# Kernel tuning notes

Hardware: AMD Instinct MI355X
Metric: run time of the kernel (lower is better)

Reference implementation:

```python
import jax, jax.numpy as jnp
import numpy as np

B, N, C = 8, 196, 512
NC, H = 10, 8
HD = C // H
SCALE = HD ** -0.5


def setup_inputs() -> dict:
    key = jax.random.key(0)
    ks = jax.random.split(key, 8)
    s = 1.0 / np.sqrt(C)
    return {
        "x": jax.random.normal(ks[0], (B, N, C), jnp.float32),
        "anchors": jax.random.normal(ks[1], (NC, N, C), jnp.float32),
        "weights": jax.random.uniform(ks[2], (B, H, NC), jnp.float32),
        "Wqk": jax.random.normal(ks[3], (C, C), jnp.float32) * s,
        "Wqk2": jax.random.normal(ks[4], (C, C), jnp.float32) * s,
        "Wv": jax.random.normal(ks[5], (C, C), jnp.float32) * s,
        "Wproj": jax.random.normal(ks[6], (C, C), jnp.float32) * s,
        "bproj": jax.random.normal(ks[7], (C,), jnp.float32) * 0.01,
    }


def _heads(t):
    # (..., N, C) -> (..., H, N, HD)
    shp = t.shape[:-2]
    return t.reshape(shp + (t.shape[-2], H, HD)).swapaxes(-3, -2)


def reference(x, anchors, weights, Wqk, Wqk2, Wv, Wproj, bproj):
    v = _heads(x @ Wv)                      # (B, H, N, HD)
    q = _heads(x @ Wqk)[:, None]            # (B, 1, H, N, HD)
    k = _heads(anchors @ Wqk)[None]         # (1, NC, H, N, HD)
    q2 = _heads(x @ Wqk2)[:, None]          # (B, 1, H, N, HD)
    k2 = _heads(anchors @ Wqk2)[None]       # (1, NC, H, N, HD)

    # ReLU-clipped double attention, both (B, NC, H, N, N)
    left_attn = jnp.maximum(-(q @ k.swapaxes(-2, -1)) * SCALE, 0.0)
    right_attn = jnp.maximum((k2 @ q2.swapaxes(-2, -1)) * SCALE, 0.0)

    attn = left_attn @ right_attn           # (B, NC, H, N, N)
    # per-head class-weighted combine: (B,H,NC) x (B,NC,H,N,N) -> (B,H,N,N)
    tmp = jnp.einsum('bhc,bchnm->bhnm', weights, attn)
    out = tmp @ v                           # (B, H, N, HD)
    # NOTE: original torch code reshapes (B,H,N,HD)->(B,N,C) WITHOUT a
    # transpose back; we replicate that exact flatten order.
    out = out.reshape(B, N, C)
    out = out @ Wproj + bproj
    return (out, left_attn)
```

## Files before the change

### kernel.cpp

```cpp
#include <hip/hip_runtime.h>

#define OFF_XB     0u
#define OFF_AB     1605632u
#define OFF_WQKT   3612672u
#define OFF_WQK2T  4136960u
#define OFF_WVT    4661248u
#define OFF_WPROJT 5185536u
#define OFF_XQ     5709824u
#define OFF_XQ2    7315456u
#define OFF_XV     8921088u
#define OFF_AQ     10526720u
#define OFF_AQ2    12533760u
#define OFF_RVT    14540800u
#define OFF_OUT1   35512320u
#define OFF_P      37117952u

typedef __attribute__((ext_vector_type(8))) short bf16x8;
typedef __attribute__((ext_vector_type(4))) float f32x4;
#define MFMA(a, b, c) __builtin_amdgcn_mfma_f32_16x16x32_bf16((a), (b), (c), 0, 0, 0)

__device__ __forceinline__ unsigned short f2bf(float x) {
  unsigned u = __builtin_bit_cast(unsigned, x);
  u += 0x7fffu + ((u >> 16) & 1u);
  return (unsigned short)(u >> 16);
}
__device__ __forceinline__ float bf2f(unsigned short s) {
  return __builtin_bit_cast(float, ((unsigned)s) << 16);
}

__device__ __forceinline__ void barrier_lds() {
  asm volatile("s_waitcnt lgkmcnt(0)" ::: "memory");
  __builtin_amdgcn_s_barrier();
  asm volatile("" ::: "memory");
}

__device__ __forceinline__ void gl_lds16(const void* g, void* l) {
  __builtin_amdgcn_global_load_lds(
      (const __attribute__((address_space(1))) unsigned int*)g,
      (__attribute__((address_space(3))) unsigned int*)l, 16, 0, 0);
}

__device__ __forceinline__ void stage64(const unsigned short* g0, int stride,
                                        unsigned short (*T)[72], int tid, int nrows) {
  int wv = tid >> 6;
  char* base = (char*)&T[0][0];
#pragma unroll
  for (int i = 0; i < 2; i++) {
    int k = i * 256 + tid;
    int r = k / 9, c = k - r * 9;
    if (r < nrows)
      gl_lds16(g0 + (size_t)r * stride + (c << 3), base + (((i << 2) + wv) << 10));
  }
  if (tid < 64) {
    int k = 512 + tid;
    int r = k / 9, c = k - r * 9;
    if (r < nrows)
      gl_lds16(g0 + (size_t)r * stride + (c << 3), base + 8192);
  }
}

__device__ __forceinline__ void stageA_f32(unsigned short (*T)[72], const float* __restrict__ A,
                                           int row0, int M, int k0, int tid) {
  int r = tid >> 2, cs = (tid & 3) << 4;
  float4 f0 = make_float4(0.f, 0.f, 0.f, 0.f), f1 = f0, f2 = f0, f3 = f0;
  if (row0 + r < M) {
    const float* p = A + (size_t)(row0 + r) * 512 + k0 + cs;
    f0 = *(const float4*)p;
    f1 = *(const float4*)(p + 4);
    f2 = *(const float4*)(p + 8);
    f3 = *(const float4*)(p + 12);
  }
  unsigned short s[16] = {f2bf(f0.x), f2bf(f0.y), f2bf(f0.z), f2bf(f0.w),
                          f2bf(f1.x), f2bf(f1.y), f2bf(f1.z), f2bf(f1.w),
                          f2bf(f2.x), f2bf(f2.y), f2bf(f2.z), f2bf(f2.w),
                          f2bf(f3.x), f2bf(f3.y), f2bf(f3.z), f2bf(f3.w)};
  *(uint4*)&T[r][cs] = *(uint4*)s;
  *(uint4*)&T[r][cs + 8] = *(uint4*)(s + 8);
}

__device__ __forceinline__ void vload_T(uint4* va, uint4* vb, const unsigned short* __restrict__ g,
                                        int row0, int nrows, int col0, int tid) {
  int j0 = tid >> 3, d0 = (tid & 7) << 3;
  *va = make_uint4(0, 0, 0, 0);
  *vb = make_uint4(0, 0, 0, 0);
  if (j0 < nrows) *va = *(const uint4*)(g + (size_t)(row0 + j0) * 512 + col0 + d0);
  if (j0 + 32 < nrows) *vb = *(const uint4*)(g + (size_t)(row0 + j0 + 32) * 512 + col0 + d0);
}
__device__ __forceinline__ void vwrite_T(unsigned short T[64][72], uint4 va, uint4 vb, int tid) {
  int j0 = tid >> 3, d0 = (tid & 7) << 3;
  int sw = (tid & 7) << 3;
  unsigned short s[8];
  *(uint4*)s = va;
#pragma unroll
  for (int u = 0; u < 8; u++) T[d0 + u][j0 ^ sw] = s[u];
  *(uint4*)s = vb;
#pragma unroll
  for (int u = 0; u < 8; u++) T[d0 + u][(j0 + 32) ^ sw] = s[u];
}

__global__ __launch_bounds__(256) void pre_kernel(const float* __restrict__ Wqk, const float* __restrict__ Wqk2,
                                                  const float* __restrict__ Wv, const float* __restrict__ Wproj,
                                                  char* __restrict__ ws) {
  __shared__ __align__(16) unsigned short Ls[64][72];
  int tid = threadIdx.x;
  int idx = blockIdx.x;
  int wsel = idx >> 6, t = idx & 63;
  int k0 = (t >> 3) << 6, n0 = (t & 7) << 6;
  const float* W;
  unsigned short* WT;
  switch (wsel) {
    case 0:  W = Wqk;   WT = (unsigned short*)(ws + OFF_WQKT);   break;
    case 1:  W = Wqk2;  WT = (unsigned short*)(ws + OFF_WQK2T);  break;
    case 2:  W = Wv;    WT = (unsigned short*)(ws + OFF_WVT);    break;
    default: W = Wproj; WT = (unsigned short*)(ws + OFF_WPROJT); break;
  }
  {
    int r = tid >> 2, seg = (tid & 3) << 4;
    const float* p = W + (size_t)(k0 + r) * 512 + n0 + seg;
    float4 f0 = *(const float4*)p, f1 = *(const float4*)(p + 4);
    float4 f2 = *(const float4*)(p + 8), f3 = *(const float4*)(p + 12);
    unsigned short s[16] = {f2bf(f0.x), f2bf(f0.y), f2bf(f0.z), f2bf(f0.w),
                            f2bf(f1.x), f2bf(f1.y), f2bf(f1.z), f2bf(f1.w),
                            f2bf(f2.x), f2bf(f2.y), f2bf(f2.z), f2bf(f2.w),
                            f2bf(f3.x), f2bf(f3.y), f2bf(f3.z), f2bf(f3.w)};
    *(uint4*)&Ls[r][seg] = *(uint4*)s;
    *(uint4*)&Ls[r][seg + 8] = *(uint4*)(s + 8);
  }
  __syncthreads();
  {
    int r = tid >> 2, seg = (tid & 3) << 4;
    unsigned short s[16];
#pragma unroll
    for (int u = 0; u < 16; u++) s[u] = Ls[seg + u][r];
    unsigned short* dst = WT + (size_t)(n0 + r) * 512 + k0 + seg;
    *(uint4*)dst = *(uint4*)s;
    *(uint4*)(dst + 8) = *(uint4*)(s + 8);
  }
}

template <int NW>
__device__ __forceinline__ void proj_body(const float* __restrict__ A,
                                          const unsigned short* W0, const unsigned short* W1,
                                          const unsigned short* W2,
                                          unsigned short* O0, unsigned short* O1, unsigned short* O2,
                                          int M, unsigned short (*As)[72], unsigned short (*Wsh)[72]) {
  int row0 = (int)blockIdx.x << 6;
  if (row0 >= M) return;
  int col0 = (int)blockIdx.y << 6;
  int tid = threadIdx.x;
  int w = tid >> 6, lm = tid & 15, lq = (tid >> 4) & 3;
  const unsigned short* WTs[3] = {W0, W1, W2};
  unsigned short* Os[3] = {O0, O1, O2};
  f32x4 acc[NW][4] = {};
  for (int k0 = 0; k0 < 512; k0 += 64) {
    __syncthreads();
    stageA_f32(As, A, row0, M, k0, tid);
#pragma unroll
    for (int ww = 0; ww < NW; ww++)
      stage64(WTs[ww] + (size_t)col0 * 512 + k0, 512,
              (unsigned short(*)[72])&Wsh[ww << 6], tid, 64);
    __syncthreads();
#pragma unroll
    for (int kk = 0; kk < 2; kk++) {
      bf16x8 af[4];
#pragma unroll
      for (int mi = 0; mi < 4; mi++)
        af[mi] = *(const bf16x8*)&As[(mi << 4) + lm][(kk << 5) + (lq << 3)];
#pragma unroll
      for (int ww = 0; ww < NW; ww++) {
        bf16x8 bf = *(const bf16x8*)&Wsh[(ww << 6) + (w << 4) + lm][(kk << 5) + (lq << 3)];
#pragma unroll
        for (int mi = 0; mi < 4; mi++) acc[ww][mi] = MFMA(af[mi], bf, acc[ww][mi]);
      }
    }
  }
  int ncol = col0 + (w << 4) + lm;
#pragma unroll
  for (int ww = 0; ww < NW; ww++)
#pragma unroll
    for (int mi = 0; mi < 4; mi++)
#pragma unroll
      for (int r2 = 0; r2 < 4; r2++) {
        int row = row0 + (mi << 4) + (lq << 2) + r2;
        if (row < M)
          Os[ww][(size_t)row * 512 + ncol] = f2bf(acc[ww][mi][r2]);
      }
}

__global__ __launch_bounds__(256) void proj_combo(const float* __restrict__ x,
                                                  const float* __restrict__ anchors,
                                                  char* __restrict__ ws) {
  __shared__ __align__(16) unsigned short As[64][72];
  __shared__ __align__(16) unsigned short Wsh[192][72];
  const unsigned short* wqkt  = (const unsigned short*)(ws + OFF_WQKT);
  const unsigned short* wqk2t = (const unsigned short*)(ws + OFF_WQK2T);
  const unsigned short* wvt   = (const unsigned short*)(ws + OFF_WVT);
  if (blockIdx.z == 0)
    proj_body<3>(x, wqkt, wqk2t, wvt,
                 (unsigned short*)(ws + OFF_XQ), (unsigned short*)(ws + OFF_XQ2),
                 (unsigned short*)(ws + OFF_XV), 1568, As, Wsh);
  else
    proj_body<2>(anchors, wqkt, wqk2t, nullptr,
                 (unsigned short*)(ws + OFF_AQ), (unsigned short*)(ws + OFF_AQ2),
                 nullptr, 1960, As, Wsh);
}

__global__ __launch_bounds__(256) void final_gemm(const unsigned short* __restrict__ out1,
                                                  const unsigned short* __restrict__ WT,
                                                  const float* __restrict__ bias, float* __restrict__ out) {
  __shared__ __align__(16) unsigned short As[64][72];
  __shared__ __align__(16) unsigned short Ws[64][72];
  int row0 = (int)blockIdx.x << 6;
  int col0 = (int)blockIdx.y << 6;
  int tid = threadIdx.x;
  int w = tid >> 6, lm = tid & 15, lq = (tid >> 4) & 3;
  f32x4 acc[4] = {};
  for (int k0 = 0; k0 < 512; k0 += 64) {
    __syncthreads();
    stage64(out1 + (size_t)row0 * 512 + k0, 512, As, tid, 64);
    stage64(WT + (size_t)col0 * 512 + k0, 512, Ws, tid, 64);
    __syncthreads();
#pragma unroll
    for (int kk = 0; kk < 2; kk++) {
      bf16x8 bf = *(const bf16x8*)&Ws[(w << 4) + lm][(kk << 5) + (lq << 3)];
#pragma unroll
      for (int mi = 0; mi < 4; mi++) {
        bf16x8 af = *(const bf16x8*)&As[(mi << 4) + lm][(kk << 5) + (lq << 3)];
        acc[mi] = MFMA(af, bf, acc[mi]);
      }
    }
  }
  int ncol = col0 + (w << 4) + lm;
  float bv = bias[ncol];
#pragma unroll
  for (int mi = 0; mi < 4; mi++)
#pragma unroll
    for (int r2 = 0; r2 < 4; r2++) {
      int row = row0 + (mi << 4) + (lq << 2) + r2;
      if (row < 1568)
        out[(size_t)row * 512 + ncol] = acc[mi][r2] + bv;
    }
}

__global__ __launch_bounds__(256) void rv_mfma(char* __restrict__ ws) {
  const unsigned short* xq2 = (const unsigned short*)(ws + OFF_XQ2);
  const unsigned short* aq2 = (const unsigned short*)(ws + OFF_AQ2);
  const unsigned short* xv  = (const unsigned short*)(ws + OFF_XV);
  unsigned short* rvt       = (unsigned short*)(ws + OFF_RVT);
  __shared__ __align__(16) unsigned short Qs[64][72];
  __shared__ __align__(16) unsigned short Vt[64][72];
  __shared__ __align__(16) unsigned short Ss[64][72];
  int d = blockIdx.x;
  int wk = ((d & 7) * 320) + (d >> 3);
  int it = wk & 3;
  int g = wk >> 2;
  int bh = g / 10, c = g - bh * 10;
  int b = bh >> 3, h = bh & 7;
  int bch = (b * 10 + c) * 8 + h;
  int i0 = it << 6;
  int tid = threadIdx.x;
  int w = tid >> 6, lm = tid & 15, lq = (tid >> 4) & 3;
  int iglob = i0 + (w << 4) + lm;

  bf16x8 kb[2] = {};
  if (iglob < 196) {
    const unsigned short* kp = aq2 + (size_t)(c * 196 + iglob) * 512 + (h << 6) + (lq << 3);
    kb[0] = *(const bf16x8*)kp;
    kb[1] = *(const bf16x8*)(kp + 32);
  }
  stage64(xq2 + (size_t)(b * 196) * 512 + (h << 6), 512, Qs, tid, 64);
  uint4 va, vb;
  vload_T(&va, &vb, xv, b * 196, 64, h << 6, tid);

  f32x4 acc[4] = {};
#pragma unroll
  for (int jt = 0; jt < 4; jt++) {
    int j0 = jt << 6;
    __syncthreads();
    vwrite_T(Vt, va, vb, tid);
    f32x4 s[4] = {};
#pragma unroll
    for (int kk = 0; kk < 2; kk++)
#pragma unroll
      for (int mj = 0; mj < 4; mj++) {
        bf16x8 af = *(const bf16x8*)&Qs[(mj << 4) + lm][(kk << 5) + (lq << 3)];
        s[mj] = MFMA(af, kb[kk], s[mj]);
      }
#pragma unroll
    for (int mj = 0; mj < 4; mj++) {
      unsigned short u[4] = {f2bf(fmaxf(0.125f * s[mj][0], 0.f)), f2bf(fmaxf(0.125f * s[mj][1], 0.f)),
                             f2bf(fmaxf(0.125f * s[mj][2], 0.f)), f2bf(fmaxf(0.125f * s[mj][3], 0.f))};
      *(uint2*)&Ss[(w << 4) + lm][(mj << 4) + (lq << 2)] = *(uint2*)u;
    }
    if (jt < 3) vload_T(&va, &vb, xv, b * 196 + j0 + 64, min(64, 196 - j0 - 64), h << 6, tid);
    barrier_lds();
    if (jt < 3) stage64(xq2 + (size_t)(b * 196 + j0 + 64) * 512 + (h << 6), 512, Qs, tid, 64);
    int vrow = (w << 4) + lm;
    int vsw = ((vrow >> 3) & 7) << 3;
#pragma unroll
    for (int kk = 0; kk < 2; kk++) {
      bf16x8 bf = *(const bf16x8*)&Vt[vrow][((kk << 5) + (lq << 3)) ^ vsw];
#pragma unroll
      for (int mi = 0; mi < 4; mi++) {
        bf16x8 af = *(const bf16x8*)&Ss[(mi << 4) + lm][(kk << 5) + (lq << 3)];
        acc[mi] = MFMA(af, bf, acc[mi]);
      }
    }
  }
  __syncthreads();
#pragma unroll
  for (int mi = 0; mi < 4; mi++) {
    unsigned short u[4] = {f2bf(acc[mi][0]), f2bf(acc[mi][1]), f2bf(acc[mi][2]), f2bf(acc[mi][3])};
    *(uint2*)&Ss[(w << 4) + lm][(mi << 4) + (lq << 2)] = *(uint2*)u;
  }
  __syncthreads();
  {
    int dd = tid >> 2, seg = (tid & 3) << 4;
    unsigned short* dst = rvt + ((size_t)(bch * 4 + it) * 64 + dd) * 64 + seg;
    *(uint4*)dst = *(uint4*)&Ss[dd][seg];
    *(uint4*)(dst + 8) = *(uint4*)&Ss[dd][seg + 8];
  }
}

__global__ __launch_bounds__(256) void attn_mfma(char* __restrict__ ws, float* __restrict__ left,
                                                 unsigned short* __restrict__ P) {
  const unsigned short* xq  = (const unsigned short*)(ws + OFF_XQ);
  const unsigned short* aq  = (const unsigned short*)(ws + OFF_AQ);
  const unsigned short* rvt = (const unsigned short*)(ws + OFF_RVT);
  __shared__ __align__(16) unsigned short Ks[64][72];
  __shared__ __align__(16) unsigned short Ss[64][72];
  int d = blockIdx.x;
  int wk = ((d & 7) * 320) + (d >> 3);
  int i0 = (wk & 3) << 6;
  int g = wk >> 2;
  int c = g >> 6;
  int bh = g & 63;
  int b = bh >> 3, h = bh & 7;
  int bch = (b * 10 + c) * 8 + h;
  int tid = threadIdx.x;
  int w = tid >> 6, lm = tid & 15, lq = (tid >> 4) & 3;
  int iglob = i0 + (w << 4) + lm;

  bf16x8 qb[2];
  {
    const unsigned short* qp = xq + (size_t)(b * 196 + iglob) * 512 + (h << 6) + (lq << 3);
    qb[0] = *(const bf16x8*)qp;
    qb[1] = *(const bf16x8*)(qp + 32);
  }
  {
    uint4 z = make_uint4(0, 0, 0, 0);
    for (int k = tid; k < 540; k += 256)
      *(uint4*)((char*)&Ks[0][0] + 576 + k * 16) = z;
  }
  stage64(aq + (size_t)(c * 196 + 192) * 512 + (h << 6), 512, Ks, tid, 4);
  const unsigned short* rbase = rvt + (size_t)bch * 16384 + (((w << 4) + lm) << 6) + (lq << 3);
  bf16x8 rv0 = *(const bf16x8*)(rbase + 3 * 4096);
  bf16x8 rv1 = *(const bf16x8*)(rbase + 3 * 4096 + 32);

  f32x4 acc[4] = {};
  size_t lbase = (size_t)bch * (196 * 196);
#pragma unroll
  for (int t = 0; t < 4; t++) {
    int jt = (t == 0) ? 3 : t - 1;
    int j0 = jt << 6;
    __syncthreads();
    f32x4 s[4] = {};
#pragma unroll
    for (int kk = 0; kk < 2; kk++)
#pragma unroll
      for (int mj = 0; mj < 4; mj++) {
        bf16x8 af = *(const bf16x8*)&Ks[(mj << 4) + lm][(kk << 5) + (lq << 3)];
        s[mj] = MFMA(af, qb[kk], s[mj]);
      }
#pragma unroll
    for (int mj = 0; mj < 4; mj++) {
      f32x4 lv;
      lv[0] = fmaxf(-0.125f * s[mj][0], 0.f);
      lv[1] = fmaxf(-0.125f * s[mj][1], 0.f);
      lv[2] = fmaxf(-0.125f * s[mj][2], 0.f);
      lv[3] = fmaxf(-0.125f * s[mj][3], 0.f);
      int jloc = (mj << 4) + (lq << 2);
      if (iglob < 196 && j0 + jloc < 196)
        *(f32x4*)&left[lbase + (size_t)iglob * 196 + j0 + jloc] = lv;
      unsigned short u[4] = {f2bf(lv[0]), f2bf(lv[1]), f2bf(lv[2]), f2bf(lv[3])};
      *(uint2*)&Ss[(w << 4) + lm][jloc] = *(uint2*)u;
    }
    barrier_lds();
    if (t < 3)
      stage64(aq + (size_t)(c * 196 + (t << 6)) * 512 + (h << 6), 512, Ks, tid, 64);
    bf16x8 cur0 = rv0, cur1 = rv1;
    if (t < 3) {
      rv0 = *(const bf16x8*)(rbase + t * 4096);
      rv1 = *(const bf16x8*)(rbase + t * 4096 + 32);
    }
#pragma unroll
    for (int kk = 0; kk < 2; kk++) {
      bf16x8 bf = (kk == 0) ? cur0 : cur1;
#pragma unroll
      for (int mi = 0; mi < 4; mi++) {
        bf16x8 af = *(const bf16x8*)&Ss[(mi << 4) + lm][(kk << 5) + (lq << 3)];
        acc[mi] = MFMA(af, bf, acc[mi]);
      }
    }
  }
  __syncthreads();
#pragma unroll
  for (int mi = 0; mi < 4; mi++)
#pragma unroll
    for (int r = 0; r < 4; r++)
      Ss[(mi << 4) + (lq << 2) + r][(w << 4) + lm] = f2bf(acc[mi][r]);
  __syncthreads();
  {
    int row = tid >> 2, seg = (tid & 3) << 4;
    if (i0 + row < 196) {
      unsigned short* dst = P + ((size_t)(bh * 10 + c) * 196 + i0 + row) * 64 + seg;
      *(uint4*)dst = *(uint4*)&Ss[row][seg];
      *(uint4*)(dst + 8) = *(uint4*)&Ss[row][seg + 8];
    }
  }
}

__global__ __launch_bounds__(256) void reduce_out1(const unsigned short* __restrict__ P,
                                                   const float* __restrict__ weights,
                                                   unsigned short* __restrict__ out1) {
  int t = blockIdx.x * 256 + threadIdx.x;
  int base = t << 2;
  int bh = base / 12544;
  int rem = base - bh * 12544;
  const float* wrow = weights + bh * 10;
  float a0 = 0.f, a1 = 0.f, a2 = 0.f, a3 = 0.f;
#pragma unroll
  for (int c = 0; c < 10; c++) {
    float wc = wrow[c];
    const unsigned short* p = P + ((size_t)(bh * 10 + c)) * 12544 + rem;
    ushort4 u = *(const ushort4*)p;
    a0 = fmaf(wc, bf2f(u.x), a0);
    a1 = fmaf(wc, bf2f(u.y), a1);
    a2 = fmaf(wc, bf2f(u.z), a2);
    a3 = fmaf(wc, bf2f(u.w), a3);
  }
  unsigned short s[4] = {f2bf(a0), f2bf(a1), f2bf(a2), f2bf(a3)};
  *(uint2*)&out1[base] = *(uint2*)s;
}

extern "C" void kernel_launch(void* const* d_in, const int* in_sizes, int n_in,
                              void* d_out, int out_size, void* d_ws, size_t ws_size,
                              hipStream_t stream) {
  (void)in_sizes; (void)n_in; (void)out_size; (void)ws_size;
  const float* x       = (const float*)d_in[0];
  const float* anchors = (const float*)d_in[1];
  const float* weights = (const float*)d_in[2];
  const float* Wqk     = (const float*)d_in[3];
  const float* Wqk2    = (const float*)d_in[4];
  const float* Wv      = (const float*)d_in[5];
  const float* Wproj   = (const float*)d_in[6];
  const float* bproj   = (const float*)d_in[7];
  char* ws = (char*)d_ws;
  float* out  = (float*)d_out;
  float* left = out + 802816;

  dim3 blk(256);
  pre_kernel<<<dim3(256), blk, 0, stream>>>(Wqk, Wqk2, Wv, Wproj, ws);
  proj_combo<<<dim3(31, 8, 2), blk, 0, stream>>>(x, anchors, ws);
  rv_mfma<<<dim3(2560), blk, 0, stream>>>(ws);
  attn_mfma<<<dim3(2560), blk, 0, stream>>>(ws, left, (unsigned short*)(ws + OFF_P));
  reduce_out1<<<dim3(784), blk, 0, stream>>>((const unsigned short*)(ws + OFF_P), weights,
                                             (unsigned short*)(ws + OFF_OUT1));
  final_gemm<<<dim3(25, 8), blk, 0, stream>>>((const unsigned short*)(ws + OFF_OUT1),
                                              (const unsigned short*)(ws + OFF_WPROJT), bproj, out);
}
```

Measured before the change: 207.5 us.

## Process two 64-row tiles per block in rv and attn kernels

Each block of rv_mfma and attn_mfma now computes two 64-row output tiles instead of one, and the grid shrinks from 2560 to 1280 blocks. The staged K/Q and V tiles in LDS and the streamed rv fragments are shared by both tiles, which halves the global-to-LDS staging traffic and the barrier count per unit of work. In exchange each block uses more registers and a larger LDS score buffer, which may lower occupancy, and there are fewer blocks to spread across the compute units.

```diff
diff --git a/kernel.cpp b/kernel.cpp
--- a/kernel.cpp
+++ b/kernel.cpp
@@ -249,48 +249,73 @@
   unsigned short* rvt       = (unsigned short*)(ws + OFF_RVT);
   __shared__ __align__(16) unsigned short Qs[64][72];
   __shared__ __align__(16) unsigned short Vt[64][72];
-  __shared__ __align__(16) unsigned short Ss[64][72];
+  __shared__ __align__(16) unsigned short Ss[128][72];
   int d = blockIdx.x;
-  int wk = ((d & 7) * 320) + (d >> 3);
-  int it = wk & 3;
-  int g = wk >> 2;
+  int wk = ((d & 7) * 160) + (d >> 3);
+  int half = wk & 1;
+  int g = wk >> 1;
   int bh = g / 10, c = g - bh * 10;
   int b = bh >> 3, h = bh & 7;
   int bch = (b * 10 + c) * 8 + h;
-  int i0 = it << 6;
+  int itA = half << 1, itB = itA + 1;
+  int i0a = itA << 6, i0b = itB << 6;
   int tid = threadIdx.x;
   int w = tid >> 6, lm = tid & 15, lq = (tid >> 4) & 3;
-  int iglob = i0 + (w << 4) + lm;
-
-  bf16x8 kb[2] = {};
-  if (iglob < 196) {
-    const unsigned short* kp = aq2 + (size_t)(c * 196 + iglob) * 512 + (h << 6) + (lq << 3);
-    kb[0] = *(const bf16x8*)kp;
-    kb[1] = *(const bf16x8*)(kp + 32);
+  int iglobA = i0a + (w << 4) + lm;
+  int iglobB = i0b + (w << 4) + lm;
+
+  bf16x8 kbA[2] = {}, kbB[2] = {};
+  {
+    const unsigned short* kpA = aq2 + (size_t)(c * 196 + iglobA) * 512 + (h << 6) + (lq << 3);
+    kbA[0] = *(const bf16x8*)kpA;
+    kbA[1] = *(const bf16x8*)(kpA + 32);
+  }
+  if (iglobB < 196) {
+    const unsigned short* kpB = aq2 + (size_t)(c * 196 + iglobB) * 512 + (h << 6) + (lq << 3);
+    kbB[0] = *(const bf16x8*)kpB;
+    kbB[1] = *(const bf16x8*)(kpB + 32);
   }
   stage64(xq2 + (size_t)(b * 196) * 512 + (h << 6), 512, Qs, tid, 64);
   uint4 va, vb;
   vload_T(&va, &vb, xv, b * 196, 64, h << 6, tid);
 
-  f32x4 acc[4] = {};
+  f32x4 accA[4] = {}, accB[4] = {};
 #pragma unroll
   for (int jt = 0; jt < 4; jt++) {
     int j0 = jt << 6;
     __syncthreads();
     vwrite_T(Vt, va, vb, tid);
-    f32x4 s[4] = {};
-#pragma unroll
-    for (int kk = 0; kk < 2; kk++)
+    {
+      f32x4 s[4] = {};
+#pragma unroll
+      for (int kk = 0; kk < 2; kk++)
+#pragma unroll
+        for (int mj = 0; mj < 4; mj++) {
+          bf16x8 af = *(const bf16x8*)&Qs[(mj << 4) + lm][(kk << 5) + (lq << 3)];
+          s[mj] = MFMA(af, kbA[kk], s[mj]);
+        }
 #pragma unroll
       for (int mj = 0; mj < 4; mj++) {
-        bf16x8 af = *(const bf16x8*)&Qs[(mj << 4) + lm][(kk << 5) + (lq << 3)];
-        s[mj] = MFMA(af, kb[kk], s[mj]);
-      }
-#pragma unroll
-    for (int mj = 0; mj < 4; mj++) {
-      unsigned short u[4] = {f2bf(fmaxf(0.125f * s[mj][0], 0.f)), f2bf(fmaxf(0.125f * s[mj][1], 0.f)),
-                             f2bf(fmaxf(0.125f * s[mj][2], 0.f)), f2bf(fmaxf(0.125f * s[mj][3], 0.f))};
-      *(uint2*)&Ss[(w << 4) + lm][(mj << 4) + (lq << 2)] = *(uint2*)u;
+        unsigned short u[4] = {f2bf(fmaxf(0.125f * s[mj][0], 0.f)), f2bf(fmaxf(0.125f * s[mj][1], 0.f)),
+                               f2bf(fmaxf(0.125f * s[mj][2], 0.f)), f2bf(fmaxf(0.125f * s[mj][3], 0.f))};
+        *(uint2*)&Ss[(w << 4) + lm][(mj << 4) + (lq << 2)] = *(uint2*)u;
+      }
+    }
+    {
+      f32x4 s[4] = {};
+#pragma unroll
+      for (int kk = 0; kk < 2; kk++)
+#pragma unroll
+        for (int mj = 0; mj < 4; mj++) {
+          bf16x8 af = *(const bf16x8*)&Qs[(mj << 4) + lm][(kk << 5) + (lq << 3)];
+          s[mj] = MFMA(af, kbB[kk], s[mj]);
+        }
+#pragma unroll
+      for (int mj = 0; mj < 4; mj++) {
+        unsigned short u[4] = {f2bf(fmaxf(0.125f * s[mj][0], 0.f)), f2bf(fmaxf(0.125f * s[mj][1], 0.f)),
+                               f2bf(fmaxf(0.125f * s[mj][2], 0.f)), f2bf(fmaxf(0.125f * s[mj][3], 0.f))};
+        *(uint2*)&Ss[64 + (w << 4) + lm][(mj << 4) + (lq << 2)] = *(uint2*)u;
+      }
     }
     if (jt < 3) vload_T(&va, &vb, xv, b * 196 + j0 + 64, min(64, 196 - j0 - 64), h << 6, tid);
     barrier_lds();
@@ -302,23 +327,33 @@
       bf16x8 bf = *(const bf16x8*)&Vt[vrow][((kk << 5) + (lq << 3)) ^ vsw];
 #pragma unroll
       for (int mi = 0; mi < 4; mi++) {
-        bf16x8 af = *(const bf16x8*)&Ss[(mi << 4) + lm][(kk << 5) + (lq << 3)];
-        acc[mi] = MFMA(af, bf, acc[mi]);
+        bf16x8 afA = *(const bf16x8*)&Ss[(mi << 4) + lm][(kk << 5) + (lq << 3)];
+        accA[mi] = MFMA(afA, bf, accA[mi]);
+      }
+#pragma unroll
+      for (int mi = 0; mi < 4; mi++) {
+        bf16x8 afB = *(const bf16x8*)&Ss[64 + (mi << 4) + lm][(kk << 5) + (lq << 3)];
+        accB[mi] = MFMA(afB, bf, accB[mi]);
       }
     }
   }
   __syncthreads();
 #pragma unroll
   for (int mi = 0; mi < 4; mi++) {
-    unsigned short u[4] = {f2bf(acc[mi][0]), f2bf(acc[mi][1]), f2bf(acc[mi][2]), f2bf(acc[mi][3])};
-    *(uint2*)&Ss[(w << 4) + lm][(mi << 4) + (lq << 2)] = *(uint2*)u;
+    unsigned short uA[4] = {f2bf(accA[mi][0]), f2bf(accA[mi][1]), f2bf(accA[mi][2]), f2bf(accA[mi][3])};
+    *(uint2*)&Ss[(w << 4) + lm][(mi << 4) + (lq << 2)] = *(uint2*)uA;
+    unsigned short uB[4] = {f2bf(accB[mi][0]), f2bf(accB[mi][1]), f2bf(accB[mi][2]), f2bf(accB[mi][3])};
+    *(uint2*)&Ss[64 + (w << 4) + lm][(mi << 4) + (lq << 2)] = *(uint2*)uB;
   }
   __syncthreads();
   {
     int dd = tid >> 2, seg = (tid & 3) << 4;
-    unsigned short* dst = rvt + ((size_t)(bch * 4 + it) * 64 + dd) * 64 + seg;
-    *(uint4*)dst = *(uint4*)&Ss[dd][seg];
-    *(uint4*)(dst + 8) = *(uint4*)&Ss[dd][seg + 8];
+    unsigned short* dstA = rvt + ((size_t)(bch * 4 + itA) * 64 + dd) * 64 + seg;
+    *(uint4*)dstA = *(uint4*)&Ss[dd][seg];
+    *(uint4*)(dstA + 8) = *(uint4*)&Ss[dd][seg + 8];
+    unsigned short* dstB = rvt + ((size_t)(bch * 4 + itB) * 64 + dd) * 64 + seg;
+    *(uint4*)dstB = *(uint4*)&Ss[64 + dd][seg];
+    *(uint4*)(dstB + 8) = *(uint4*)&Ss[64 + dd][seg + 8];
   }
 }
 
@@ -328,24 +363,29 @@
   const unsigned short* aq  = (const unsigned short*)(ws + OFF_AQ);
   const unsigned short* rvt = (const unsigned short*)(ws + OFF_RVT);
   __shared__ __align__(16) unsigned short Ks[64][72];
-  __shared__ __align__(16) unsigned short Ss[64][72];
+  __shared__ __align__(16) unsigned short Ss[128][72];
   int d = blockIdx.x;
-  int wk = ((d & 7) * 320) + (d >> 3);
-  int i0 = (wk & 3) << 6;
-  int g = wk >> 2;
+  int wk = ((d & 7) * 160) + (d >> 3);
+  int half = wk & 1;
+  int g = wk >> 1;
   int c = g >> 6;
   int bh = g & 63;
   int b = bh >> 3, h = bh & 7;
   int bch = (b * 10 + c) * 8 + h;
+  int i0a = half << 7, i0b = i0a + 64;
   int tid = threadIdx.x;
   int w = tid >> 6, lm = tid & 15, lq = (tid >> 4) & 3;
-  int iglob = i0 + (w << 4) + lm;
-
-  bf16x8 qb[2];
-  {
-    const unsigned short* qp = xq + (size_t)(b * 196 + iglob) * 512 + (h << 6) + (lq << 3);
-    qb[0] = *(const bf16x8*)qp;
-    qb[1] = *(const bf16x8*)(qp + 32);
+  int iglobA = i0a + (w << 4) + lm;
+  int iglobB = i0b + (w << 4) + lm;
+
+  bf16x8 qbA[2], qbB[2];
+  {
+    const unsigned short* qpA = xq + (size_t)(b * 196 + iglobA) * 512 + (h << 6) + (lq << 3);
+    qbA[0] = *(const bf16x8*)qpA;
+    qbA[1] = *(const bf16x8*)(qpA + 32);
+    const unsigned short* qpB = xq + (size_t)(b * 196 + iglobB) * 512 + (h << 6) + (lq << 3);
+    qbB[0] = *(const bf16x8*)qpB;
+    qbB[1] = *(const bf16x8*)(qpB + 32);
   }
   {
     uint4 z = make_uint4(0, 0, 0, 0);
@@ -357,33 +397,58 @@
   bf16x8 rv0 = *(const bf16x8*)(rbase + 3 * 4096);
   bf16x8 rv1 = *(const bf16x8*)(rbase + 3 * 4096 + 32);
 
-  f32x4 acc[4] = {};
+  f32x4 accA[4] = {}, accB[4] = {};
   size_t lbase = (size_t)bch * (196 * 196);
 #pragma unroll
   for (int t = 0; t < 4; t++) {
     int jt = (t == 0) ? 3 : t - 1;
     int j0 = jt << 6;
     __syncthreads();
-    f32x4 s[4] = {};
-#pragma unroll
-    for (int kk = 0; kk < 2; kk++)
+    {
+      f32x4 s[4] = {};
+#pragma unroll
+      for (int kk = 0; kk < 2; kk++)
+#pragma unroll
+        for (int mj = 0; mj < 4; mj++) {
+          bf16x8 af = *(const bf16x8*)&Ks[(mj << 4) + lm][(kk << 5) + (lq << 3)];
+          s[mj] = MFMA(af, qbA[kk], s[mj]);
+        }
 #pragma unroll
       for (int mj = 0; mj < 4; mj++) {
-        bf16x8 af = *(const bf16x8*)&Ks[(mj << 4) + lm][(kk << 5) + (lq << 3)];
-        s[mj] = MFMA(af, qb[kk], s[mj]);
-      }
-#pragma unroll
-    for (int mj = 0; mj < 4; mj++) {
-      f32x4 lv;
-      lv[0] = fmaxf(-0.125f * s[mj][0], 0.f);
-      lv[1] = fmaxf(-0.125f * s[mj][1], 0.f);
-      lv[2] = fmaxf(-0.125f * s[mj][2], 0.f);
-      lv[3] = fmaxf(-0.125f * s[mj][3], 0.f);
-      int jloc = (mj << 4) + (lq << 2);
-      if (iglob < 196 && j0 + jloc < 196)
-        *(f32x4*)&left[lbase + (size_t)iglob * 196 + j0 + jloc] = lv;
-      unsigned short u[4] = {f2bf(lv[0]), f2bf(lv[1]), f2bf(lv[2]), f2bf(lv[3])};
-      *(uint2*)&Ss[(w << 4) + lm][jloc] = *(uint2*)u;
+        f32x4 lv;
+        lv[0] = fmaxf(-0.125f * s[mj][0], 0.f);
+        lv[1] = fmaxf(-0.125f * s[mj][1], 0.f);
+        lv[2] = fmaxf(-0.125f * s[mj][2], 0.f);
+        lv[3] = fmaxf(-0.125f * s[mj][3], 0.f);
+        int jloc = (mj << 4) + (lq << 2);
+        if (iglobA < 196 && j0 + jloc < 196)
+          *(f32x4*)&left[lbase + (size_t)iglobA * 196 + j0 + jloc] = lv;
+        unsigned short u[4] = {f2bf(lv[0]), f2bf(lv[1]), f2bf(lv[2]), f2bf(lv[3])};
+        *(uint2*)&Ss[(w << 4) + lm][jloc] = *(uint2*)u;
+      }
+    }
+    {
+      f32x4 s[4] = {};
+#pragma unroll
+      for (int kk = 0; kk < 2; kk++)
+#pragma unroll
+        for (int mj = 0; mj < 4; mj++) {
+          bf16x8 af = *(const bf16x8*)&Ks[(mj << 4) + lm][(kk << 5) + (lq << 3)];
+          s[mj] = MFMA(af, qbB[kk], s[mj]);
+        }
+#pragma unroll
+      for (int mj = 0; mj < 4; mj++) {
+        f32x4 lv;
+        lv[0] = fmaxf(-0.125f * s[mj][0], 0.f);
+        lv[1] = fmaxf(-0.125f * s[mj][1], 0.f);
+        lv[2] = fmaxf(-0.125f * s[mj][2], 0.f);
+        lv[3] = fmaxf(-0.125f * s[mj][3], 0.f);
+        int jloc = (mj << 4) + (lq << 2);
+        if (iglobB < 196 && j0 + jloc < 196)
+          *(f32x4*)&left[lbase + (size_t)iglobB * 196 + j0 + jloc] = lv;
+        unsigned short u[4] = {f2bf(lv[0]), f2bf(lv[1]), f2bf(lv[2]), f2bf(lv[3])};
+        *(uint2*)&Ss[64 + (w << 4) + lm][jloc] = *(uint2*)u;
+      }
     }
     barrier_lds();
     if (t < 3)
@@ -398,8 +463,13 @@
       bf16x8 bf = (kk == 0) ? cur0 : cur1;
 #pragma unroll
       for (int mi = 0; mi < 4; mi++) {
-        bf16x8 af = *(const bf16x8*)&Ss[(mi << 4) + lm][(kk << 5) + (lq << 3)];
-        acc[mi] = MFMA(af, bf, acc[mi]);
+        bf16x8 afA = *(const bf16x8*)&Ss[(mi << 4) + lm][(kk << 5) + (lq << 3)];
+        accA[mi] = MFMA(afA, bf, accA[mi]);
+      }
+#pragma unroll
+      for (int mi = 0; mi < 4; mi++) {
+        bf16x8 afB = *(const bf16x8*)&Ss[64 + (mi << 4) + lm][(kk << 5) + (lq << 3)];
+        accB[mi] = MFMA(afB, bf, accB[mi]);
       }
     }
   }
@@ -407,15 +477,20 @@
 #pragma unroll
   for (int mi = 0; mi < 4; mi++)
 #pragma unroll
-    for (int r = 0; r < 4; r++)
-      Ss[(mi << 4) + (lq << 2) + r][(w << 4) + lm] = f2bf(acc[mi][r]);
+    for (int r = 0; r < 4; r++) {
+      Ss[(mi << 4) + (lq << 2) + r][(w << 4) + lm] = f2bf(accA[mi][r]);
+      Ss[64 + (mi << 4) + (lq << 2) + r][(w << 4) + lm] = f2bf(accB[mi][r]);
+    }
   __syncthreads();
   {
     int row = tid >> 2, seg = (tid & 3) << 4;
-    if (i0 + row < 196) {
-      unsigned short* dst = P + ((size_t)(bh * 10 + c) * 196 + i0 + row) * 64 + seg;
-      *(uint4*)dst = *(uint4*)&Ss[row][seg];
-      *(uint4*)(dst + 8) = *(uint4*)&Ss[row][seg + 8];
+    unsigned short* dstA = P + ((size_t)(bh * 10 + c) * 196 + i0a + row) * 64 + seg;
+    *(uint4*)dstA = *(uint4*)&Ss[row][seg];
+    *(uint4*)(dstA + 8) = *(uint4*)&Ss[row][seg + 8];
+    if (i0b + row < 196) {
+      unsigned short* dstB = P + ((size_t)(bh * 10 + c) * 196 + i0b + row) * 64 + seg;
+      *(uint4*)dstB = *(uint4*)&Ss[64 + row][seg];
+      *(uint4*)(dstB + 8) = *(uint4*)&Ss[64 + row][seg + 8];
     }
   }
 }
@@ -462,8 +537,8 @@
   dim3 blk(256);
   pre_kernel<<<dim3(256), blk, 0, stream>>>(Wqk, Wqk2, Wv, Wproj, ws);
   proj_combo<<<dim3(31, 8, 2), blk, 0, stream>>>(x, anchors, ws);
-  rv_mfma<<<dim3(2560), blk, 0, stream>>>(ws);
-  attn_mfma<<<dim3(2560), blk, 0, stream>>>(ws, left, (unsigned short*)(ws + OFF_P));
+  rv_mfma<<<dim3(1280), blk, 0, stream>>>(ws);
+  attn_mfma<<<dim3(1280), blk, 0, stream>>>(ws, left, (unsigned short*)(ws + OFF_P));
   reduce_out1<<<dim3(784), blk, 0, stream>>>((const unsigned short*)(ws + OFF_P), weights,
                                              (unsigned short*)(ws + OFF_OUT1));
   final_gemm<<<dim3(25, 8), blk, 0, stream>>>((const unsigned short*)(ws + OFF_OUT1),
```

Result: no change. 207.7 us (+0.1%).
